# Performance work log

Measured on AMD Instinct MI355X. Metric: run time of the kernel, lower is better.

The kernel has to match this reference:

```python
import jax, jax.numpy as jnp
import numpy as np

EPS = 1e-8


def setup_inputs() -> dict:
    key = jax.random.key(0)
    pred_softmax = jax.random.uniform(key, (16, 11, 1, 512, 512), dtype=jnp.float32)
    return {"pred_softmax": pred_softmax}


def reference(pred_softmax):
    B, P, C, H, W = pred_softmax.shape
    # view(B, P, H, W) then drop last part channel
    x = pred_softmax.reshape(B, P, H, W)[:, : P - 1]  # [B, P-1, H, W]
    # coordinate maps (square maps assumed by original code): x_map varies along
    # columns, y_map along rows, both normalized to [-1, 1)
    x_map = (jnp.arange(W, dtype=x.dtype) / W * 2.0 - 1.0)[None, :]   # [1, W]
    y_map = (jnp.arange(H, dtype=x.dtype) / H * 2.0 - 1.0)[:, None]   # [H, 1]
    # per-(b,c) normalization to a pdf
    k = x.sum(axis=(-2, -1), keepdims=True) + EPS
    pdf = x / k                                                       # [B, P-1, H, W]
    # weighted centroids
    x_c = (pdf * x_map).sum(axis=(-2, -1))                            # [B, P-1]
    y_c = (pdf * y_map).sum(axis=(-2, -1))                            # [B, P-1]
    # weighted variances around the centroid
    dx2 = (x_map[None, None] - x_c[..., None, None]) ** 2             # [B, P-1, 1 or H, W]
    dy2 = (y_map[None, None] - y_c[..., None, None]) ** 2
    v_x = (pdf * dx2).sum(axis=(-2, -1))
    v_y = (pdf * dy2).sum(axis=(-2, -1))
    loss = (v_x + v_y).sum() / B
    return loss
```

## Files before the change

### kernel.cpp

```cpp
#include <hip/hip_runtime.h>

#define HH 512
#define WW 512
#define NPART 11
#define NP 10
#define NB 16
#define NBP (NB * NP)
#define CHUNKS 8
#define ROWS_PER_CHUNK (HH / CHUNKS)
#define BLOCK 256
#define F4_PER_CHUNK (ROWS_PER_CHUNK * WW / 4)
#define ITERS (F4_PER_CHUNK / BLOCK)

__global__ __launch_bounds__(BLOCK) void partial_kernel(
    const float* __restrict__ in, float* __restrict__ ws) {
  const int blk = blockIdx.x;
  const int bp = blk / CHUNKS;
  const int chunk = blk - bp * CHUNKS;
  const int b = bp / NP;
  const int p = bp - b * NP;

  const float4* __restrict__ in4 =
      (const float4*)(in + ((size_t)(b * NPART + p) * HH +
                            (size_t)chunk * ROWS_PER_CHUNK) * WW);
  const int t = threadIdx.x;

  float s = 0.f, sx = 0.f, sy = 0.f, sx2 = 0.f, sy2 = 0.f;
  const float inv256 = 1.0f / 256.0f;

  #pragma unroll 4
  for (int j = 0; j < ITERS; ++j) {
    const int fi = j * BLOCK + t;
    const float4 v = in4[fi];
    const int row = fi >> 7;
    const int w0 = (fi & 127) << 2;
    const float ym = (float)(chunk * ROWS_PER_CHUNK + row) * inv256 - 1.0f;
    const float xm0 = (float)w0 * inv256 - 1.0f;
    const float xm1 = xm0 + inv256;
    const float xm2 = xm0 + 2.0f * inv256;
    const float xm3 = xm0 + 3.0f * inv256;

    const float sum4 = (v.x + v.y) + (v.z + v.w);
    s += sum4;
    sy = fmaf(ym, sum4, sy);
    sy2 = fmaf(ym * ym, sum4, sy2);
    sx = fmaf(v.x, xm0, sx);
    sx = fmaf(v.y, xm1, sx);
    sx = fmaf(v.z, xm2, sx);
    sx = fmaf(v.w, xm3, sx);
    sx2 = fmaf(v.x, xm0 * xm0, sx2);
    sx2 = fmaf(v.y, xm1 * xm1, sx2);
    sx2 = fmaf(v.z, xm2 * xm2, sx2);
    sx2 = fmaf(v.w, xm3 * xm3, sx2);
  }

  #pragma unroll
  for (int off = 32; off > 0; off >>= 1) {
    s   += __shfl_xor(s, off);
    sx  += __shfl_xor(sx, off);
    sy  += __shfl_xor(sy, off);
    sx2 += __shfl_xor(sx2, off);
    sy2 += __shfl_xor(sy2, off);
  }

  __shared__ float red[BLOCK / 64][5];
  const int wave = t >> 6;
  const int lane = t & 63;
  if (lane == 0) {
    red[wave][0] = s;
    red[wave][1] = sx;
    red[wave][2] = sy;
    red[wave][3] = sx2;
    red[wave][4] = sy2;
  }
  __syncthreads();
  if (t < 5) {
    float acc = red[0][t] + red[1][t] + red[2][t] + red[3][t];
    ws[(size_t)blk * 5 + t] = acc;
  }
}

__global__ __launch_bounds__(BLOCK) void finalize_kernel(
    const float* __restrict__ ws, float* __restrict__ out) {
  const int t = threadIdx.x;
  float c = 0.f;
  if (t < NBP) {
    float S = 0.f, Sx = 0.f, Sy = 0.f, Sx2 = 0.f, Sy2 = 0.f;
    #pragma unroll
    for (int ch = 0; ch < CHUNKS; ++ch) {
      const float* q = ws + (size_t)(t * CHUNKS + ch) * 5;
      S   += q[0];
      Sx  += q[1];
      Sy  += q[2];
      Sx2 += q[3];
      Sy2 += q[4];
    }
    const float k = S + 1e-8f;
    const float inv = 1.0f / k;
    const float xc = Sx * inv;
    const float yc = Sy * inv;
    const float vx = (Sx2 - 2.0f * xc * Sx + xc * xc * S) * inv;
    const float vy = (Sy2 - 2.0f * yc * Sy + yc * yc * S) * inv;
    c = vx + vy;
  }

  #pragma unroll
  for (int off = 32; off > 0; off >>= 1) {
    c += __shfl_xor(c, off);
  }

  __shared__ float red[BLOCK / 64];
  const int wave = t >> 6;
  const int lane = t & 63;
  if (lane == 0) red[wave] = c;
  __syncthreads();
  if (t == 0) {
    float total = red[0] + red[1] + red[2] + red[3];
    out[0] = total * (1.0f / (float)NB);
  }
}

extern "C" void kernel_launch(void* const* d_in, const int* in_sizes, int n_in,
                              void* d_out, int out_size, void* d_ws, size_t ws_size,
                              hipStream_t stream) {
  const float* in = (const float*)d_in[0];
  float* out = (float*)d_out;
  float* ws = (float*)d_ws;

  partial_kernel<<<NBP * CHUNKS, BLOCK, 0, stream>>>(in, ws);
  finalize_kernel<<<1, BLOCK, 0, stream>>>(ws, out);
}
```

Baseline: 247.9 us.

## Double chunk count, hoist per-thread column weights, and load two float4s per iteration

```diff
diff --git a/kernel.cpp b/kernel.cpp
--- a/kernel.cpp
+++ b/kernel.cpp
@@ -6,11 +6,11 @@
 #define NP 10
 #define NB 16
 #define NBP (NB * NP)
-#define CHUNKS 8
+#define CHUNKS 16
 #define ROWS_PER_CHUNK (HH / CHUNKS)
 #define BLOCK 256
 #define F4_PER_CHUNK (ROWS_PER_CHUNK * WW / 4)
-#define ITERS (F4_PER_CHUNK / BLOCK)
+#define ITERS (F4_PER_CHUNK / (BLOCK * 2))
 
 __global__ __launch_bounds__(BLOCK) void partial_kernel(
     const float* __restrict__ in, float* __restrict__ ws) {
@@ -24,34 +24,46 @@
       (const float4*)(in + ((size_t)(b * NPART + p) * HH +
                             (size_t)chunk * ROWS_PER_CHUNK) * WW);
   const int t = threadIdx.x;
+  const float inv256 = 1.0f / 256.0f;
+
+  const int w0 = (t & 127) << 2;
+  const float xm0 = (float)w0 * inv256 - 1.0f;
+  const float xm1 = xm0 + inv256;
+  const float xm2 = xm0 + 2.0f * inv256;
+  const float xm3 = xm0 + 3.0f * inv256;
+  const float xq0 = xm0 * xm0, xq1 = xm1 * xm1, xq2 = xm2 * xm2, xq3 = xm3 * xm3;
 
   float s = 0.f, sx = 0.f, sy = 0.f, sx2 = 0.f, sy2 = 0.f;
-  const float inv256 = 1.0f / 256.0f;
 
-  #pragma unroll 4
+  #pragma unroll
   for (int j = 0; j < ITERS; ++j) {
-    const int fi = j * BLOCK + t;
-    const float4 v = in4[fi];
-    const int row = fi >> 7;
-    const int w0 = (fi & 127) << 2;
-    const float ym = (float)(chunk * ROWS_PER_CHUNK + row) * inv256 - 1.0f;
-    const float xm0 = (float)w0 * inv256 - 1.0f;
-    const float xm1 = xm0 + inv256;
-    const float xm2 = xm0 + 2.0f * inv256;
-    const float xm3 = xm0 + 3.0f * inv256;
+    const int fi0 = (j * 2) * BLOCK + t;
+    const int fi1 = fi0 + BLOCK;
+    const float4 v0 = in4[fi0];
+    const float4 v1 = in4[fi1];
 
-    const float sum4 = (v.x + v.y) + (v.z + v.w);
-    s += sum4;
-    sy = fmaf(ym, sum4, sy);
-    sy2 = fmaf(ym * ym, sum4, sy2);
-    sx = fmaf(v.x, xm0, sx);
-    sx = fmaf(v.y, xm1, sx);
-    sx = fmaf(v.z, xm2, sx);
-    sx = fmaf(v.w, xm3, sx);
-    sx2 = fmaf(v.x, xm0 * xm0, sx2);
-    sx2 = fmaf(v.y, xm1 * xm1, sx2);
-    sx2 = fmaf(v.z, xm2 * xm2, sx2);
-    sx2 = fmaf(v.w, xm3 * xm3, sx2);
+    const int row0 = fi0 >> 7;
+    const int row1 = fi1 >> 7;
+    const float ym0 = (float)(chunk * ROWS_PER_CHUNK + row0) * inv256 - 1.0f;
+    const float ym1 = (float)(chunk * ROWS_PER_CHUNK + row1) * inv256 - 1.0f;
+
+    const float sum0 = (v0.x + v0.y) + (v0.z + v0.w);
+    const float sum1 = (v1.x + v1.y) + (v1.z + v1.w);
+    s += sum0 + sum1;
+    sy = fmaf(ym0, sum0, sy);
+    sy = fmaf(ym1, sum1, sy);
+    sy2 = fmaf(ym0 * ym0, sum0, sy2);
+    sy2 = fmaf(ym1 * ym1, sum1, sy2);
+
+    sx = fmaf(v0.x, xm0, sx);  sx = fmaf(v0.y, xm1, sx);
+    sx = fmaf(v0.z, xm2, sx);  sx = fmaf(v0.w, xm3, sx);
+    sx = fmaf(v1.x, xm0, sx);  sx = fmaf(v1.y, xm1, sx);
+    sx = fmaf(v1.z, xm2, sx);  sx = fmaf(v1.w, xm3, sx);
+
+    sx2 = fmaf(v0.x, xq0, sx2);  sx2 = fmaf(v0.y, xq1, sx2);
+    sx2 = fmaf(v0.z, xq2, sx2);  sx2 = fmaf(v0.w, xq3, sx2);
+    sx2 = fmaf(v1.x, xq0, sx2);  sx2 = fmaf(v1.y, xq1, sx2);
+    sx2 = fmaf(v1.z, xq2, sx2);  sx2 = fmaf(v1.w, xq3, sx2);
   }
 
   #pragma unroll
```

Result: no change. 246.4 us (-0.6%).
